# Kernel tuning notes

Hardware: AMD Instinct MI355X
Metric: run time of the kernel (lower is better)

## Reference

```python
import jax, jax.numpy as jnp
import numpy as np

D_MODEL = 2048
N_HEADS = 16
HEAD_DIM = D_MODEL // N_HEADS
D_FF = 8192
B, T = 2, 2048
LN_EPS = 1e-5


def layer_norm(x, g, b):
    mu = jnp.mean(x, axis=-1, keepdims=True)
    var = jnp.mean(jnp.square(x - mu), axis=-1, keepdims=True)
    return (x - mu) * jax.lax.rsqrt(var + LN_EPS) * g + b


def setup_inputs() -> dict:
    key = jax.random.key(0)
    ks = jax.random.split(key, 8)
    s = 0.02
    return {
        "x": jax.random.normal(ks[0], (B, T, D_MODEL), dtype=jnp.float32),
        "ln1_g": jnp.ones((D_MODEL,), jnp.float32),
        "ln1_b": jnp.zeros((D_MODEL,), jnp.float32),
        "ln2_g": jnp.ones((D_MODEL,), jnp.float32),
        "ln2_b": jnp.zeros((D_MODEL,), jnp.float32),
        "w_qkv": jax.random.normal(ks[1], (3 * D_MODEL, D_MODEL), jnp.float32) * s,
        "w_out": jax.random.normal(ks[2], (D_MODEL, D_MODEL), jnp.float32) * s,
        "w_up": jax.random.normal(ks[3], (D_FF, D_MODEL), jnp.float32) * s,
        "b_up": jnp.zeros((D_FF,), jnp.float32),
        "w_down": jax.random.normal(ks[4], (D_MODEL, D_FF), jnp.float32) * s,
        "b_down": jnp.zeros((D_MODEL,), jnp.float32),
    }


def reference(x, ln1_g, ln1_b, ln2_g, ln2_b, w_qkv, w_out, w_up, b_up, w_down, b_down):
    b, t, c = x.shape
    # --- attention (pre-norm) ---
    h = layer_norm(x, ln1_g, ln1_b)
    qkv = h @ w_qkv.T                                  # [B,T,3C]
    q, k, v = jnp.split(qkv, 3, axis=-1)
    # [B,H,T,Dh]
    q = q.reshape(b, t, N_HEADS, HEAD_DIM).transpose(0, 2, 1, 3)
    k = k.reshape(b, t, N_HEADS, HEAD_DIM).transpose(0, 2, 1, 3)
    v = v.reshape(b, t, N_HEADS, HEAD_DIM).transpose(0, 2, 1, 3)
    scale = 1.0 / np.sqrt(HEAD_DIM).astype(np.float32)
    attn = jnp.einsum("bhqd,bhkd->bhqk", q, k) * scale
    causal = jnp.tril(jnp.ones((t, t), dtype=bool))
    attn = jnp.where(causal, attn, jnp.float32(-jnp.inf))
    attn = jax.nn.softmax(attn, axis=-1)
    out = jnp.einsum("bhqk,bhkd->bhqd", attn, v)
    out = out.transpose(0, 2, 1, 3).reshape(b, t, c)
    x = x + out @ w_out.T
    # --- FFN (pre-norm, GeLU exact) ---
    h = layer_norm(x, ln2_g, ln2_b)
    h = jax.nn.gelu(h @ w_up.T + b_up, approximate=False)
    x = x + h @ w_down.T + b_down
    return x
```

## Files before the change

### kernel.cpp

```cpp
#include <hip/hip_runtime.h>
#include <cstdint>
#include <cstddef>

using u16 = unsigned short;
typedef __attribute__((ext_vector_type(8))) __bf16 bf16x8;
typedef __attribute__((ext_vector_type(4))) float f32x4;

__device__ inline u16 f2bf(float f) {
  union { float f; unsigned u; } v; v.f = f;
  unsigned r = (v.u + 0x7fffu + ((v.u >> 16) & 1u)) >> 16;
  return (u16)r;
}

__device__ inline float bf2f(u16 u) {
  union { unsigned u; float f; } v; v.u = (unsigned)u << 16;
  return v.f;
}

#define GLDS(g, s) __builtin_amdgcn_global_load_lds( \
    (__attribute__((address_space(1))) void*)(g), \
    (__attribute__((address_space(3))) void*)(s), 16, 0, 0)

__global__ __launch_bounds__(256) void cvt_all(const float* __restrict__ a0,
                                               const float* __restrict__ a1,
                                               const float* __restrict__ a2,
                                               const float* __restrict__ a3,
                                               u16* __restrict__ o0, u16* __restrict__ o1,
                                               u16* __restrict__ o2, u16* __restrict__ o3) {
  int stride = gridDim.x * 256;
  for (int i = blockIdx.x * 256 + threadIdx.x; i < 6291456; i += stride) {
    const float* in; u16* out; int j = i;
    if (j < 1572864) { in = a0; out = o0; }
    else if ((j -= 1572864) < 524288) { in = a1; out = o1; }
    else if ((j -= 524288) < 2097152) { in = a2; out = o2; }
    else { j -= 2097152; in = a3; out = o3; }
    float4 v0 = *(const float4*)&in[(size_t)j * 8];
    float4 v1 = *(const float4*)&in[(size_t)j * 8 + 4];
    union { u16 u[8]; uint4 q; } pk;
    pk.u[0] = f2bf(v0.x); pk.u[1] = f2bf(v0.y); pk.u[2] = f2bf(v0.z); pk.u[3] = f2bf(v0.w);
    pk.u[4] = f2bf(v1.x); pk.u[5] = f2bf(v1.y); pk.u[6] = f2bf(v1.z); pk.u[7] = f2bf(v1.w);
    *(uint4*)&out[(size_t)j * 8] = pk.q;
  }
}

__global__ __launch_bounds__(256) void ln_bf16(const float* __restrict__ x,
                                               const float* __restrict__ g,
                                               const float* __restrict__ bsh,
                                               u16* __restrict__ out) {
  __shared__ float red[8];
  int tid = threadIdx.x;
  int lane = tid & 63, w = tid >> 6;
  size_t row = blockIdx.x;
  const float* xr = x + row * 2048;
  float4 v0 = *(const float4*)&xr[tid * 8];
  float4 v1 = *(const float4*)&xr[tid * 8 + 4];
  float s = v0.x + v0.y + v0.z + v0.w + v1.x + v1.y + v1.z + v1.w;
  float s2 = v0.x*v0.x + v0.y*v0.y + v0.z*v0.z + v0.w*v0.w
           + v1.x*v1.x + v1.y*v1.y + v1.z*v1.z + v1.w*v1.w;
#pragma unroll
  for (int m = 1; m < 64; m <<= 1) { s += __shfl_xor(s, m); s2 += __shfl_xor(s2, m); }
  if (lane == 0) { red[w] = s; red[w + 4] = s2; }
  __syncthreads();
  s = red[0] + red[1] + red[2] + red[3];
  s2 = red[4] + red[5] + red[6] + red[7];
  float mu = s * (1.0f / 2048.0f);
  float var = s2 * (1.0f / 2048.0f) - mu * mu;
  float rs = rsqrtf(var + 1e-5f);
  float4 g0 = *(const float4*)&g[tid * 8];
  float4 g1 = *(const float4*)&g[tid * 8 + 4];
  float4 b0 = *(const float4*)&bsh[tid * 8];
  float4 b1 = *(const float4*)&bsh[tid * 8 + 4];
  float xv[8] = {v0.x, v0.y, v0.z, v0.w, v1.x, v1.y, v1.z, v1.w};
  float gv[8] = {g0.x, g0.y, g0.z, g0.w, g1.x, g1.y, g1.z, g1.w};
  float bv[8] = {b0.x, b0.y, b0.z, b0.w, b1.x, b1.y, b1.z, b1.w};
  union { u16 u[8]; uint4 q; } pk;
#pragma unroll
  for (int j = 0; j < 8; j++) pk.u[j] = f2bf((xv[j] - mu) * rs * gv[j] + bv[j]);
  *(uint4*)&out[row * 2048 + tid * 8] = pk.q;
}

__global__ __launch_bounds__(256) void combine4h(const u16* __restrict__ p,
                                                 const float* __restrict__ resid,
                                                 const float* __restrict__ bias,
                                                 float* __restrict__ out, int n8) {
  int stride = gridDim.x * 256;
  for (int i = blockIdx.x * 256 + threadIdx.x; i < n8; i += stride) {
    size_t base = (size_t)i * 8;
    float s[8];
    float4 r0 = *(const float4*)&resid[base];
    float4 r1 = *(const float4*)&resid[base + 4];
    s[0]=r0.x; s[1]=r0.y; s[2]=r0.z; s[3]=r0.w;
    s[4]=r1.x; s[5]=r1.y; s[6]=r1.z; s[7]=r1.w;
    if (bias) {
      int col0 = (int)(base & 2047);
      float4 b0 = *(const float4*)&bias[col0];
      float4 b1 = *(const float4*)&bias[col0 + 4];
      s[0]+=b0.x; s[1]+=b0.y; s[2]+=b0.z; s[3]+=b0.w;
      s[4]+=b1.x; s[5]+=b1.y; s[6]+=b1.z; s[7]+=b1.w;
    }
#pragma unroll
    for (int k = 0; k < 4; ++k) {
      union { uint4 q; u16 u[8]; } v;
      v.q = *(const uint4*)&p[(size_t)k * 8388608 + base];
#pragma unroll
      for (int j = 0; j < 8; ++j) s[j] += bf2f(v.u[j]);
    }
    float4 o0 = {s[0], s[1], s[2], s[3]};
    float4 o1 = {s[4], s[5], s[6], s[7]};
    *(float4*)&out[base] = o0;
    *(float4*)&out[base + 4] = o1;
  }
}

template <int EPI, int LDK, int KLEN, int NSPLIT>
__global__ __launch_bounds__(512, 4) void gemm_bk32(
    const u16* __restrict__ A, const u16* __restrict__ B,
    int M, int N, const float* __restrict__ bias, u16* __restrict__ outh,
    int xc, int chr, int chc) {
  __shared__ u16 lds[36864];
  constexpr int NT = KLEN / 32;
  int tid = threadIdx.x;
  int lane = tid & 63, wid = tid >> 6;
  int wr = wid >> 2, wc = wid & 3;
  int lr = lane & 15, lg = lane >> 4;

  unsigned dly = (blockIdx.x * 2654435761u) >> 29;
  for (unsigned i = 0; i < dly; ++i) asm volatile("s_sleep 6" ::: "memory");

  int sub = blockIdx.x;
  if (NSPLIT > 1) {
    int per = (M >> 7) * (N >> 8);
    int ks = sub / per;
    sub -= ks * per;
    A += (size_t)ks * KLEN;
    B += (size_t)ks * KLEN;
    outh += (size_t)ks * M * N;
  }
  int xcd = sub & 7, slot = sub >> 3;
  int rr = slot / chc, cc = slot - rr * chc;
  int by = (xcd / xc) * chr + rr;
  int bx = (xcd - (xcd / xc) * xc) * chc + cc;
  size_t bm = (size_t)by * 128, bn = (size_t)bx * 256;

  const u16* Ablk = A + bm * LDK;
  const u16* Bblk = B + bn * LDK;

  int sA = (tid >> 2) * LDK + (((tid & 3) ^ ((tid >> 3) & 3)) * 8);
  int gs = (lg ^ ((lr >> 1) & 3)) * 8;
  int aoff = (wr * 64 + lr) * 32 + gs;
  int boff = 4096 + (wc * 64 + lr) * 32 + gs;

  f32x4 acc[4][4];
#pragma unroll
  for (int mq = 0; mq < 4; ++mq)
#pragma unroll
    for (int nq = 0; nq < 4; ++nq) acc[mq][nq] = (f32x4){0.f, 0.f, 0.f, 0.f};

  bf16x8 af[4], bfr[4];

#define STAGE(bb, tt) do { \
    const u16* As = Ablk + (tt) * 32 + sA; \
    const u16* Bs = Bblk + (tt) * 32 + sA; \
    GLDS(As, &lds[(bb) * 12288 + tid * 8]); \
    GLDS(Bs, &lds[(bb) * 12288 + 4096 + tid * 8]); \
    GLDS(Bs + 128 * (size_t)LDK, &lds[(bb) * 12288 + 8192 + tid * 8]); \
  } while (0)
#define BARS do { __builtin_amdgcn_s_barrier(); __builtin_amdgcn_sched_barrier(0); } while (0)

  STAGE(0, 0);
  STAGE(1, 1);

  int c = 0;
  for (int t = 0; t < NT; ++t) {
    if (t + 1 < NT) {
      asm volatile("s_waitcnt vmcnt(3)" ::: "memory");
    } else {
      asm volatile("s_waitcnt vmcnt(0)" ::: "memory");
    }
    BARS;
#pragma unroll
    for (int mq = 0; mq < 4; ++mq)
      af[mq] = *(const bf16x8*)&lds[c * 12288 + mq * 512 + aoff];
#pragma unroll
    for (int nq = 0; nq < 4; ++nq)
      bfr[nq] = *(const bf16x8*)&lds[c * 12288 + nq * 512 + boff];
    if (t + 2 < NT) {
      int cs = c + 2; if (cs >= 3) cs -= 3;
      STAGE(cs, t + 2);
    }
    __builtin_amdgcn_s_setprio(1);
#pragma unroll
    for (int mq = 0; mq < 4; ++mq)
#pragma unroll
      for (int nq = 0; nq < 4; ++nq)
        acc[mq][nq] = __builtin_amdgcn_mfma_f32_16x16x32_bf16(af[mq], bfr[nq], acc[mq][nq], 0, 0, 0);
    __builtin_amdgcn_s_setprio(0);
    c = (c == 2) ? 0 : c + 1;
  }

#undef STAGE
#undef BARS

  size_t row0 = bm + wr * 64, col0 = bn + wc * 64;
#pragma unroll
  for (int mq = 0; mq < 4; ++mq) {
#pragma unroll
    for (int nq = 0; nq < 4; ++nq) {
#pragma unroll
      for (int r = 0; r < 4; ++r) {
        size_t row = row0 + mq * 16 + lg * 4 + r;
        size_t col = col0 + nq * 16 + lr;
        size_t idx = row * (size_t)N + col;
        float v = acc[mq][nq][r];
        if (EPI == 0) {
          outh[idx] = f2bf(v);
        } else {
          v += bias[col];
          outh[idx] = f2bf(0.5f * v * (1.0f + erff(v * 0.70710678118654752f)));
        }
      }
    }
  }
}

__global__ __launch_bounds__(256) void vtrans(const u16* __restrict__ qkv,
                                              u16* __restrict__ vt) {
  __shared__ u16 tile[32][33];
  int tx = threadIdx.x & 31, ty = threadIdx.x >> 5;
  int t0 = blockIdx.x * 32, d0 = blockIdx.y * 32, bh = blockIdx.z;
  int b = bh >> 4, h = bh & 15;
  const u16* src = qkv + (size_t)b * 2048 * 6144 + 4096 + h * 128 + d0;
#pragma unroll
  for (int i = 0; i < 4; i++)
    tile[ty + i * 8][tx] = src[(size_t)(t0 + ty + i * 8) * 6144 + tx];
  __syncthreads();
  u16* dst = vt + (size_t)bh * 128 * 2048 + (size_t)d0 * 2048 + t0;
#pragma unroll
  for (int i = 0; i < 4; i++)
    dst[(size_t)(ty + i * 8) * 2048 + tx] = tile[tx][ty + i * 8];
}

__device__ inline void stage_kv(const u16* __restrict__ ktok, const u16* __restrict__ vbase,
                                int k0, u16* kb, u16* vb, int tid) {
#pragma unroll
  for (int c = 0; c < 4; ++c) {
    int s = c * 256 + tid;
    int r = s >> 4, g = s & 15;
    const u16* src = ktok + (size_t)(k0 + r) * 6144 + ((g ^ (r & 7)) * 8);
    GLDS(src, &kb[s * 8]);
  }
#pragma unroll
  for (int c = 0; c < 4; ++c) {
    int s = c * 256 + tid;
    int d = s >> 3, g = s & 7;
    const u16* src = vbase + (size_t)d * 2048 + k0 + ((g ^ (d & 7)) * 8);
    GLDS(src, &vb[s * 8]);
  }
}

__global__ __launch_bounds__(256) void attn_fwd(const u16* __restrict__ qkv,
                                                const u16* __restrict__ vt,
                                                u16* __restrict__ outh) {
  __shared__ u16 kbuf[2][8192];
  __shared__ u16 vbuf[2][8192];
  __shared__ u16 p_lds[4][1024];
  int tid = threadIdx.x, lane = tid & 63, w = tid >> 6;
  int lr = lane & 15, lg = lane >> 4;
  int bh = blockIdx.x, p = blockIdx.y;
  int b = bh >> 4, h = bh & 15;
  const float scale = 0.08838834764831845f;
  const u16* tokbase = qkv + (size_t)b * 2048 * 6144;
  const u16* ktok = tokbase + 2048 + h * 128;
  const u16* vbase = vt + (size_t)bh * 262144;
  u16* pl = p_lds[w];

  for (int half = 0; half < 2; ++half) {
    int qt = (half == 0) ? p : 31 - p;
    int qbase = qt * 64 + w * 16;
    int nt = qt + 1;

    bf16x8 qf[4];
    const u16* qrow_ptr = tokbase + (size_t)(qbase + lr) * 6144 + h * 128;
#pragma unroll
    for (int kk = 0; kk < 4; kk++) qf[kk] = *(const bf16x8*)&qrow_ptr[kk * 32 + lg * 8];

    f32x4 o[8];
#pragma unroll
    for (int d = 0; d < 8; d++) o[d] = (f32x4){0.f, 0.f, 0.f, 0.f};
    float mrow[4] = {-1e30f, -1e30f, -1e30f, -1e30f};
    float lsum[4] = {0.f, 0.f, 0.f, 0.f};

    int cur = 0;
    stage_kv(ktok, vbase, 0, kbuf[0], vbuf[0], tid);
    __syncthreads();

    for (int t = 0; t < nt; ++t) {
      int k0 = t * 64;
      if (t + 1 < nt) stage_kv(ktok, vbase, k0 + 64, kbuf[cur ^ 1], vbuf[cur ^ 1], tid);
      const u16* kb = kbuf[cur];
      const u16* vb = vbuf[cur];

      f32x4 s[4];
#pragma unroll
      for (int c = 0; c < 4; c++) s[c] = (f32x4){0.f, 0.f, 0.f, 0.f};
#pragma unroll
      for (int kk = 0; kk < 4; kk++) {
#pragma unroll
        for (int c = 0; c < 4; c++) {
          bf16x8 kf = *(const bf16x8*)&kb[(c * 16 + lr) * 128 + (((kk * 4 + lg) ^ (lr & 7)) * 8)];
          s[c] = __builtin_amdgcn_mfma_f32_16x16x32_bf16(qf[kk], kf, s[c], 0, 0, 0);
        }
      }

      float mt[4];
#pragma unroll
      for (int r = 0; r < 4; r++) {
        int qrow = qbase + lg * 4 + r;
        float m = -1e30f;
#pragma unroll
        for (int c = 0; c < 4; c++) {
          int key = k0 + c * 16 + lr;
          float v = (key <= qrow) ? s[c][r] * scale : -1e30f;
          s[c][r] = v;
          m = fmaxf(m, v);
        }
        mt[r] = m;
      }
#pragma unroll
      for (int msk = 1; msk < 16; msk <<= 1)
#pragma unroll
        for (int r = 0; r < 4; r++) mt[r] = fmaxf(mt[r], __shfl_xor(mt[r], msk));
      float al[4], ps[4];
#pragma unroll
      for (int r = 0; r < 4; r++) {
        float mn = fmaxf(mrow[r], mt[r]);
        al[r] = __expf(mrow[r] - mn);
        mrow[r] = mn;
        float sum = 0.f;
#pragma unroll
        for (int c = 0; c < 4; c++) {
          float pv = __expf(s[c][r] - mn);
          s[c][r] = pv;
          sum += pv;
        }
        ps[r] = sum;
      }
#pragma unroll
      for (int msk = 1; msk < 16; msk <<= 1)
#pragma unroll
        for (int r = 0; r < 4; r++) ps[r] += __shfl_xor(ps[r], msk);
#pragma unroll
      for (int r = 0; r < 4; r++) lsum[r] = lsum[r] * al[r] + ps[r];
#pragma unroll
      for (int d = 0; d < 8; d++)
#pragma unroll
        for (int r = 0; r < 4; r++) o[d][r] *= al[r];

#pragma unroll
      for (int r = 0; r < 4; r++) {
        int prow = lg * 4 + r;
#pragma unroll
        for (int c = 0; c < 4; c++) {
          int gw = (c * 2 + (lr >> 3)) ^ (prow & 7);
          pl[prow * 64 + gw * 8 + (lr & 7)] = f2bf(s[c][r]);
        }
      }
      asm volatile("s_waitcnt lgkmcnt(0)" ::: "memory");
      bf16x8 pa[2];
#pragma unroll
      for (int ks = 0; ks < 2; ks++)
        pa[ks] = *(const bf16x8*)&pl[lr * 64 + (((ks * 4 + lg) ^ (lr & 7)) * 8)];
#pragma unroll
      for (int dt = 0; dt < 8; dt++) {
#pragma unroll
        for (int ks = 0; ks < 2; ks++) {
          bf16x8 vf = *(const bf16x8*)&vb[(dt * 16 + lr) * 64 + (((ks * 4 + lg) ^ (lr & 7)) * 8)];
          o[dt] = __builtin_amdgcn_mfma_f32_16x16x32_bf16(pa[ks], vf, o[dt], 0, 0, 0);
        }
      }
      __syncthreads();
      cur ^= 1;
    }

    float inv[4];
#pragma unroll
    for (int r = 0; r < 4; r++) inv[r] = 1.0f / lsum[r];
    u16* ob = outh + (size_t)(b * 2048 + qbase) * 2048 + h * 128;
#pragma unroll
    for (int dt = 0; dt < 8; dt++)
#pragma unroll
      for (int r = 0; r < 4; r++)
        ob[(size_t)(lg * 4 + r) * 2048 + dt * 16 + lr] = f2bf(o[dt][r] * inv[r]);
  }
}

extern "C" void kernel_launch(void* const* d_in, const int* in_sizes, int n_in,
                              void* d_out, int out_size, void* d_ws, size_t ws_size,
                              hipStream_t stream) {
  const float* x      = (const float*)d_in[0];
  const float* ln1_g  = (const float*)d_in[1];
  const float* ln1_b  = (const float*)d_in[2];
  const float* ln2_g  = (const float*)d_in[3];
  const float* ln2_b  = (const float*)d_in[4];
  const float* w_qkv  = (const float*)d_in[5];
  const float* w_out  = (const float*)d_in[6];
  const float* w_up   = (const float*)d_in[7];
  const float* b_up   = (const float*)d_in[8];
  const float* w_down = (const float*)d_in[9];
  const float* b_down = (const float*)d_in[10];
  float* outp = (float*)d_out;

  char* ws = (char*)d_ws;
  u16* w_qkv_bf  = (u16*)(ws + 0);
  u16* w_out_bf  = (u16*)(ws + 25165824);
  u16* w_up_bf   = (u16*)(ws + 33554432);
  u16* w_down_bf = (u16*)(ws + 67108864);
  u16* hb        = (u16*)(ws + 100663296);
  u16* qkvb      = (u16*)(ws + 117440512);
  u16* vtb       = (u16*)(ws + 167772160);
  u16* ub        = (u16*)(ws + 117440512);
  float* x1      = (float*)(ws + 184549376);
  u16* oPartH    = (u16*)(ws + 117440512);
  u16* dPartH    = (u16*)(ws + 0);

  cvt_all<<<4096, 256, 0, stream>>>(w_qkv, w_out, w_up, w_down,
                                    w_qkv_bf, w_out_bf, w_up_bf, w_down_bf);

  ln_bf16<<<4096, 256, 0, stream>>>(x, ln1_g, ln1_b, hb);
  gemm_bk32<0, 2048, 2048, 1><<<768, 512, 0, stream>>>(hb, w_qkv_bf, 4096, 6144,
                                                       nullptr, qkvb, 4, 16, 6);
  vtrans<<<dim3(64, 4, 32), 256, 0, stream>>>(qkvb, vtb);
  attn_fwd<<<dim3(32, 16), 256, 0, stream>>>(qkvb, vtb, hb);
  gemm_bk32<0, 2048, 512, 4><<<1024, 512, 0, stream>>>(hb, w_out_bf, 4096, 2048,
                                                       nullptr, oPartH, 2, 8, 4);
  combine4h<<<2048, 256, 0, stream>>>(oPartH, x, nullptr, x1, 1048576);

  ln_bf16<<<4096, 256, 0, stream>>>(x1, ln2_g, ln2_b, hb);
  gemm_bk32<2, 2048, 2048, 1><<<1024, 512, 0, stream>>>(hb, w_up_bf, 4096, 8192,
                                                        b_up, ub, 4, 16, 8);
  gemm_bk32<0, 8192, 2048, 4><<<1024, 512, 0, stream>>>(ub, w_down_bf, 4096, 2048,
                                                        nullptr, dPartH, 2, 8, 4);
  combine4h<<<2048, 256, 0, stream>>>(dPartH, x1, b_down, outp, 1048576);
}
```

Measured before the change: 637.4 us.

## Halve split-K for out/down projections and fuse combine with LayerNorm

The out-projection and down-projection GEMMs now split K two ways instead of four, with grids shrunk from 1024 to 512 blocks, so each partial buffer is read half as often. The combine after the out projection is fused with the second LayerNorm, which writes x1 and the bf16 normalized rows in one pass and removes a separate kernel and a re-read of x1. The cost is fewer blocks for the two GEMMs, which may lower occupancy and load balance on the many CUs of the device.

```diff
diff --git a/kernel.cpp b/kernel.cpp
--- a/kernel.cpp
+++ b/kernel.cpp
@@ -79,36 +79,72 @@
   *(uint4*)&out[row * 2048 + tid * 8] = pk.q;
 }
 
-__global__ __launch_bounds__(256) void combine4h(const u16* __restrict__ p,
+__global__ __launch_bounds__(256) void combineLN(const u16* __restrict__ p,
+                                                 const float* __restrict__ resid,
+                                                 const float* __restrict__ g,
+                                                 const float* __restrict__ bsh,
+                                                 float* __restrict__ x1,
+                                                 u16* __restrict__ hb) {
+  __shared__ float red[8];
+  int tid = threadIdx.x, lane = tid & 63, w = tid >> 6;
+  size_t row = blockIdx.x;
+  size_t base = row * 2048 + tid * 8;
+  union { uint4 q; u16 u[8]; } a, b;
+  a.q = *(const uint4*)&p[base];
+  b.q = *(const uint4*)&p[8388608 + base];
+  float4 r0 = *(const float4*)&resid[base];
+  float4 r1 = *(const float4*)&resid[base + 4];
+  float v[8] = {r0.x, r0.y, r0.z, r0.w, r1.x, r1.y, r1.z, r1.w};
+  float s = 0.f, s2 = 0.f;
+#pragma unroll
+  for (int j = 0; j < 8; ++j) {
+    v[j] += bf2f(a.u[j]) + bf2f(b.u[j]);
+    s += v[j]; s2 += v[j] * v[j];
+  }
+  *(float4*)&x1[base] = (float4){v[0], v[1], v[2], v[3]};
+  *(float4*)&x1[base + 4] = (float4){v[4], v[5], v[6], v[7]};
+#pragma unroll
+  for (int m = 1; m < 64; m <<= 1) { s += __shfl_xor(s, m); s2 += __shfl_xor(s2, m); }
+  if (lane == 0) { red[w] = s; red[w + 4] = s2; }
+  __syncthreads();
+  s = red[0] + red[1] + red[2] + red[3];
+  s2 = red[4] + red[5] + red[6] + red[7];
+  float mu = s * (1.0f / 2048.0f);
+  float var = s2 * (1.0f / 2048.0f) - mu * mu;
+  float rs = rsqrtf(var + 1e-5f);
+  float4 g0 = *(const float4*)&g[tid * 8];
+  float4 g1 = *(const float4*)&g[tid * 8 + 4];
+  float4 b0 = *(const float4*)&bsh[tid * 8];
+  float4 b1 = *(const float4*)&bsh[tid * 8 + 4];
+  float gv[8] = {g0.x, g0.y, g0.z, g0.w, g1.x, g1.y, g1.z, g1.w};
+  float bv[8] = {b0.x, b0.y, b0.z, b0.w, b1.x, b1.y, b1.z, b1.w};
+  union { u16 u[8]; uint4 q; } pk;
+#pragma unroll
+  for (int j = 0; j < 8; j++) pk.u[j] = f2bf((v[j] - mu) * rs * gv[j] + bv[j]);
+  *(uint4*)&hb[base] = pk.q;
+}
+
+__global__ __launch_bounds__(256) void combine2f(const u16* __restrict__ p,
                                                  const float* __restrict__ resid,
                                                  const float* __restrict__ bias,
                                                  float* __restrict__ out, int n8) {
   int stride = gridDim.x * 256;
   for (int i = blockIdx.x * 256 + threadIdx.x; i < n8; i += stride) {
     size_t base = (size_t)i * 8;
-    float s[8];
+    union { uint4 q; u16 u[8]; } a, b;
+    a.q = *(const uint4*)&p[base];
+    b.q = *(const uint4*)&p[8388608 + base];
     float4 r0 = *(const float4*)&resid[base];
     float4 r1 = *(const float4*)&resid[base + 4];
-    s[0]=r0.x; s[1]=r0.y; s[2]=r0.z; s[3]=r0.w;
-    s[4]=r1.x; s[5]=r1.y; s[6]=r1.z; s[7]=r1.w;
-    if (bias) {
-      int col0 = (int)(base & 2047);
-      float4 b0 = *(const float4*)&bias[col0];
-      float4 b1 = *(const float4*)&bias[col0 + 4];
-      s[0]+=b0.x; s[1]+=b0.y; s[2]+=b0.z; s[3]+=b0.w;
-      s[4]+=b1.x; s[5]+=b1.y; s[6]+=b1.z; s[7]+=b1.w;
-    }
-#pragma unroll
-    for (int k = 0; k < 4; ++k) {
-      union { uint4 q; u16 u[8]; } v;
-      v.q = *(const uint4*)&p[(size_t)k * 8388608 + base];
-#pragma unroll
-      for (int j = 0; j < 8; ++j) s[j] += bf2f(v.u[j]);
-    }
-    float4 o0 = {s[0], s[1], s[2], s[3]};
-    float4 o1 = {s[4], s[5], s[6], s[7]};
-    *(float4*)&out[base] = o0;
-    *(float4*)&out[base + 4] = o1;
+    int col0 = (int)(base & 2047);
+    float4 bb0 = *(const float4*)&bias[col0];
+    float4 bb1 = *(const float4*)&bias[col0 + 4];
+    float v[8] = {r0.x + bb0.x, r0.y + bb0.y, r0.z + bb0.z, r0.w + bb0.w,
+                  r1.x + bb1.x, r1.y + bb1.y, r1.z + bb1.z, r1.w + bb1.w};
+#pragma unroll
+    for (int j = 0; j < 8; ++j) v[j] += bf2f(a.u[j]) + bf2f(b.u[j]);
+    *(float4*)&out[base] = (float4){v[0], v[1], v[2], v[3]};
+    *(float4*)&out[base + 4] = (float4){v[4], v[5], v[6], v[7]};
   }
 }
 
@@ -431,14 +467,13 @@
                                                        nullptr, qkvb, 4, 16, 6);
   vtrans<<<dim3(64, 4, 32), 256, 0, stream>>>(qkvb, vtb);
   attn_fwd<<<dim3(32, 16), 256, 0, stream>>>(qkvb, vtb, hb);
-  gemm_bk32<0, 2048, 512, 4><<<1024, 512, 0, stream>>>(hb, w_out_bf, 4096, 2048,
+  gemm_bk32<0, 2048, 1024, 2><<<512, 512, 0, stream>>>(hb, w_out_bf, 4096, 2048,
                                                        nullptr, oPartH, 2, 8, 4);
-  combine4h<<<2048, 256, 0, stream>>>(oPartH, x, nullptr, x1, 1048576);
-
-  ln_bf16<<<4096, 256, 0, stream>>>(x1, ln2_g, ln2_b, hb);
+  combineLN<<<4096, 256, 0, stream>>>(oPartH, x, ln2_g, ln2_b, x1, hb);
+
   gemm_bk32<2, 2048, 2048, 1><<<1024, 512, 0, stream>>>(hb, w_up_bf, 4096, 8192,
                                                         b_up, ub, 4, 16, 8);
-  gemm_bk32<0, 8192, 2048, 4><<<1024, 512, 0, stream>>>(ub, w_down_bf, 4096, 2048,
-                                                        nullptr, dPartH, 2, 8, 4);
-  combine4h<<<2048, 256, 0, stream>>>(dPartH, x1, b_down, outp, 1048576);
-}
+  gemm_bk32<0, 8192, 4096, 2><<<512, 512, 0, stream>>>(ub, w_down_bf, 4096, 2048,
+                                                       nullptr, dPartH, 2, 8, 4);
+  combine2f<<<2048, 256, 0, stream>>>(dPartH, x1, b_down, outp, 1048576);
+}
```

Result: faster. 621.2 us, median of 4 (-2.5%).
